# Kernel optimization log

Measured on AMD Instinct MI355X. Metric: run time of the kernel, lower is better.

## Reference

```python
import jax, jax.numpy as jnp
import numpy as np

N, IN_DIM, H1, H2, LIN, MAX_INDEX = 16384, 64, 256, 256, 64, 256


def _init_layer(key, out_dim, in_dim):
    # mimic kaiming_uniform(a=sqrt(5)) + uniform bias bound = 1/sqrt(fan_in)
    kW, kb = jax.random.split(key)
    bound_w = 1.0 / np.sqrt(in_dim)  # gain*sqrt(3/fan_in) with a=sqrt(5) -> 1/sqrt(fan_in)
    W = jax.random.uniform(kW, (MAX_INDEX, out_dim, in_dim), jnp.float32, -bound_w, bound_w)
    b = jax.random.uniform(kb, (MAX_INDEX, out_dim), jnp.float32, -bound_w, bound_w)
    return W, b


def setup_inputs() -> dict:
    key = jax.random.key(0)
    kx, ki, k1, k2, k3 = jax.random.split(key, 5)
    x = jax.random.normal(kx, (N, IN_DIM), jnp.float32)
    ind = jax.random.randint(ki, (N,), 0, MAX_INDEX, jnp.int64 if jax.config.jax_enable_x64 else jnp.int32)
    W1, b1 = _init_layer(k1, H1, IN_DIM)
    W2, b2 = _init_layer(k2, H2, H1)
    Wl, bl = _init_layer(k3, LIN, H2)
    return {"x": x, "ind": ind, "W1": W1, "b1": b1, "W2": W2, "b2": b2, "Wl": Wl, "bl": bl}


def _index_linear(x, ind, W, b):
    # per-row expert weight gather then row-wise matvec: out[n] = W[ind[n]] @ x[n] + b[ind[n]]
    return jnp.einsum('noi,ni->no', W[ind], x) + b[ind]


def reference(x, ind, W1, b1, W2, b2, Wl, bl):
    h = jnp.tanh(_index_linear(x, ind, W1, b1))
    h = jnp.tanh(_index_linear(h, ind, W2, b2))
    return _index_linear(h, ind, Wl, bl)
```

## Files before the change

kernel.cpp:

```cpp
#include <hip/hip_runtime.h>
#include <math.h>

#define NROWS   16384
#define IN_DIM  64
#define HID     256
#define OUT_DIM 64
#define NEXP    256
#define MT      64
#define HP      264

typedef __attribute__((ext_vector_type(8))) short short8;
typedef __attribute__((ext_vector_type(4))) float f32x4;
typedef __attribute__((ext_vector_type(4))) unsigned uint4v;
typedef __attribute__((ext_vector_type(2))) unsigned uint2v;


__global__ __launch_bounds__(1024) void prep_k(const int* __restrict__ ind,
                                               int* __restrict__ rows,
                                               int* __restrict__ offsets) {
  __shared__ int hist[NEXP];
  __shared__ int scan[NEXP];
  __shared__ int cur[NEXP];
  int t = threadIdx.x;
  if (t < NEXP) hist[t] = 0;
  __syncthreads();
  for (int n = t; n < NROWS; n += 1024) atomicAdd(&hist[ind[n]], 1);
  __syncthreads();
  if (t < NEXP) scan[t] = hist[t];
  __syncthreads();
  for (int d = 1; d < NEXP; d <<= 1) {
    int v = (t < NEXP && t >= d) ? scan[t - d] : 0;
    __syncthreads();
    if (t < NEXP) scan[t] += v;
    __syncthreads();
  }
  if (t < NEXP) {
    int exc = scan[t] - hist[t];
    offsets[t] = exc;
    cur[t] = exc;
    if (t == NEXP - 1) offsets[NEXP] = scan[t];
  }
  __syncthreads();
  for (int n = t; n < NROWS; n += 1024) {
    int p = atomicAdd(&cur[ind[n]], 1);
    rows[p] = n;
  }
}


__device__ __forceinline__ unsigned bf16_rn(float f) {
  unsigned u = __builtin_bit_cast(unsigned, f);
  unsigned r = 0x7fffu + ((u >> 16) & 1u);
  return (u + r) >> 16;
}

__device__ __forceinline__ unsigned pk2(float a, float b) {
  return bf16_rn(a) | (bf16_rn(b) << 16);
}

__device__ __forceinline__ short8 cvt8(f32x4 w0, f32x4 w1) {
  uint4v u;
  u.x = pk2(w0.x, w0.y);
  u.y = pk2(w0.z, w0.w);
  u.z = pk2(w1.x, w1.y);
  u.w = pk2(w1.z, w1.w);
  return __builtin_bit_cast(short8, u);
}

__device__ __forceinline__ float fast_tanh(float v) {
  float e = __expf(2.f * v);
  return 1.f - 2.f * __builtin_amdgcn_rcpf(e + 1.f);
}

template <int K, int NMT>
__device__ __forceinline__ void layer_mm(const float* __restrict__ Wp,
                                         const float* __restrict__ bp,
                                         const unsigned short* Hin,
                                         int l15, int q, f32x4 (&acc)[NMT][4]) {
#pragma unroll
  for (int mt = 0; mt < NMT; mt++) {
    f32x4 bv = *(const f32x4*)(bp + mt * 16 + q * 4);
#pragma unroll
    for (int nt = 0; nt < 4; nt++) acc[mt][nt] = bv;
  }
  const float* wr[NMT];
#pragma unroll
  for (int mt = 0; mt < NMT; mt++)
    wr[mt] = Wp + (size_t)(mt * 16 + l15) * K + q * 8;

#pragma unroll 2
  for (int ks = 0; ks < K / 32; ks++) {
    short8 bfr[4];
#pragma unroll
    for (int nt = 0; nt < 4; nt++)
      bfr[nt] = *(const short8*)&Hin[(nt * 16 + l15) * HP + ks * 32 + q * 8];
#pragma unroll
    for (int mt = 0; mt < NMT; mt++) {
      f32x4 w0 = *(const f32x4*)(wr[mt] + ks * 32);
      f32x4 w1 = *(const f32x4*)(wr[mt] + ks * 32 + 4);
      short8 a = cvt8(w0, w1);
#pragma unroll
      for (int nt = 0; nt < 4; nt++)
        acc[mt][nt] =
            __builtin_amdgcn_mfma_f32_16x16x32_bf16(a, bfr[nt], acc[mt][nt], 0, 0, 0);
    }
  }
}

__device__ __forceinline__ void write_h(f32x4 (&acc)[4][4], unsigned short* H,
                                        int w, int l15, int q) {
#pragma unroll
  for (int mt = 0; mt < 4; mt++)
#pragma unroll
    for (int nt = 0; nt < 4; nt++) {
      uint2v v;
      v.x = pk2(fast_tanh(acc[mt][nt].x), fast_tanh(acc[mt][nt].y));
      v.y = pk2(fast_tanh(acc[mt][nt].z), fast_tanh(acc[mt][nt].w));
      *(uint2v*)&H[(nt * 16 + l15) * HP + w * 64 + mt * 16 + q * 4] = v;
    }
}


__global__ __launch_bounds__(256, 2) void mlp_k(
    const float* __restrict__ x,
    const float* __restrict__ W1, const float* __restrict__ b1,
    const float* __restrict__ W2, const float* __restrict__ b2,
    const float* __restrict__ Wl, const float* __restrict__ bl,
    const int* __restrict__ rows, const int* __restrict__ offsets,
    float* __restrict__ out) {
  __shared__ __align__(16) unsigned short H[MT * HP];

  const int t = threadIdx.x;
  const int w = t >> 6;
  const int l15 = t & 15;
  const int q = (t >> 4) & 3;
  const int e = blockIdx.x >> 1;
  const int j = blockIdx.x & 1;
  const int beg = offsets[e];
  const int cnt = offsets[e + 1] - beg;

  const float* W1e = W1 + (size_t)e * HID * IN_DIM + (size_t)(w * 64) * IN_DIM;
  const float* W2e = W2 + (size_t)e * HID * HID + (size_t)(w * 64) * HID;
  const float* Wle = Wl + (size_t)e * OUT_DIM * HID + (size_t)(w * 16) * HID;
  const float* b1e = b1 + e * HID + w * 64;
  const float* b2e = b2 + e * HID + w * 64;
  const float* ble = bl + e * OUT_DIM + w * 16;

  const int sm = t >> 2;
  const int sc = (t & 3) * 16;

  for (int mt0 = j * MT; mt0 < cnt; mt0 += 2 * MT) {
    __syncthreads();
    {
      int gm = mt0 + sm;
      bool val = gm < cnt;
      int r = val ? rows[beg + gm] : 0;
      const float* xr = x + (size_t)r * IN_DIM + sc;
      uint4v u0, u1;
      if (val) {
        f32x4 a0 = *(const f32x4*)(xr);
        f32x4 a1 = *(const f32x4*)(xr + 4);
        f32x4 a2 = *(const f32x4*)(xr + 8);
        f32x4 a3 = *(const f32x4*)(xr + 12);
        u0.x = pk2(a0.x, a0.y); u0.y = pk2(a0.z, a0.w);
        u0.z = pk2(a1.x, a1.y); u0.w = pk2(a1.z, a1.w);
        u1.x = pk2(a2.x, a2.y); u1.y = pk2(a2.z, a2.w);
        u1.z = pk2(a3.x, a3.y); u1.w = pk2(a3.z, a3.w);
      } else {
        u0 = (uint4v){0, 0, 0, 0};
        u1 = (uint4v){0, 0, 0, 0};
      }
      *(uint4v*)&H[sm * HP + sc] = u0;
      *(uint4v*)&H[sm * HP + sc + 8] = u1;
    }
    __syncthreads();

    {
      f32x4 acc[4][4];
      layer_mm<IN_DIM, 4>(W1e, b1e, H, l15, q, acc);
      __syncthreads();
      write_h(acc, H, w, l15, q);
    }
    __syncthreads();

    {
      f32x4 acc[4][4];
      layer_mm<HID, 4>(W2e, b2e, H, l15, q, acc);
      __syncthreads();
      write_h(acc, H, w, l15, q);
    }
    __syncthreads();

    {
      f32x4 acc[1][4];
      layer_mm<HID, 1>(Wle, ble, H, l15, q, acc);
#pragma unroll
      for (int nt = 0; nt < 4; nt++) {
        int gm = mt0 + nt * 16 + l15;
        if (gm < cnt) {
          int r = rows[beg + gm];
          *(f32x4*)(out + (size_t)r * OUT_DIM + w * 16 + q * 4) = acc[0][nt];
        }
      }
    }
  }
}


extern "C" void kernel_launch(void* const* d_in, const int* in_sizes, int n_in,
                              void* d_out, int out_size, void* d_ws, size_t ws_size,
                              hipStream_t stream) {
  const float* x   = (const float*)d_in[0];
  const int*   ind = (const int*)d_in[1];
  const float* W1  = (const float*)d_in[2];
  const float* b1  = (const float*)d_in[3];
  const float* W2  = (const float*)d_in[4];
  const float* b2  = (const float*)d_in[5];
  const float* Wl  = (const float*)d_in[6];
  const float* bl  = (const float*)d_in[7];
  float* out = (float*)d_out;

  int* offsets = (int*)d_ws;
  int* rows    = (int*)d_ws + 260;

  prep_k<<<1, 1024, 0, stream>>>(ind, rows, offsets);
  mlp_k<<<NEXP * 2, 256, 0, stream>>>(x, W1, b1, W2, b2, Wl, bl, rows, offsets, out);
}
```

Measured before the change: 170.7 us.

## Shrink row tile to 32, prefetch weights, truncate weight bf16 conversion

Halves the per-block row tile from 64 to 32, so experts with about 64 rows get both blocks busy instead of one idling. Weight loads are software-prefetched one k-step ahead with a fully unrolled loop, weights are converted to bf16 by truncation instead of manual rounding, and activations use the HIP bf16 intrinsic. Blocks are reordered so the two halves of one expert are 256 apart in launch order. The trade-off is that each block now reloads the full expert weights for half as many rows, the prefetch raises register use, and truncating weights adds some error.

```diff
diff --git a/kernel.cpp b/kernel.cpp
--- a/kernel.cpp
+++ b/kernel.cpp
@@ -1,4 +1,5 @@
 #include <hip/hip_runtime.h>
+#include <hip/hip_bf16.h>
 #include <math.h>
 
 #define NROWS   16384
@@ -6,7 +7,7 @@
 #define HID     256
 #define OUT_DIM 64
 #define NEXP    256
-#define MT      64
+#define MT      32
 #define HP      264
 
 typedef __attribute__((ext_vector_type(8))) short short8;
@@ -48,22 +49,25 @@
 }
 
 
-__device__ __forceinline__ unsigned bf16_rn(float f) {
-  unsigned u = __builtin_bit_cast(unsigned, f);
-  unsigned r = 0x7fffu + ((u >> 16) & 1u);
-  return (u + r) >> 16;
-}
-
-__device__ __forceinline__ unsigned pk2(float a, float b) {
-  return bf16_rn(a) | (bf16_rn(b) << 16);
-}
-
-__device__ __forceinline__ short8 cvt8(f32x4 w0, f32x4 w1) {
+__device__ __forceinline__ unsigned pk2_trunc(float a, float b) {
+  unsigned ua = __builtin_bit_cast(unsigned, a);
+  unsigned ub = __builtin_bit_cast(unsigned, b);
+  return (ub & 0xffff0000u) | (ua >> 16);
+}
+
+__device__ __forceinline__ unsigned pk2_rn(float a, float b) {
+  __hip_bfloat162 h = __float22bfloat162_rn(float2{a, b});
+  unsigned r;
+  __builtin_memcpy(&r, &h, 4);
+  return r;
+}
+
+__device__ __forceinline__ short8 cvt8w(f32x4 w0, f32x4 w1) {
   uint4v u;
-  u.x = pk2(w0.x, w0.y);
-  u.y = pk2(w0.z, w0.w);
-  u.z = pk2(w1.x, w1.y);
-  u.w = pk2(w1.z, w1.w);
+  u.x = pk2_trunc(w0.x, w0.y);
+  u.y = pk2_trunc(w0.z, w0.w);
+  u.z = pk2_trunc(w1.x, w1.y);
+  u.w = pk2_trunc(w1.z, w1.w);
   return __builtin_bit_cast(short8, u);
 }
 
@@ -72,50 +76,67 @@
   return 1.f - 2.f * __builtin_amdgcn_rcpf(e + 1.f);
 }
 
-template <int K, int NMT>
+template <int K, int NMT, int NNT>
 __device__ __forceinline__ void layer_mm(const float* __restrict__ Wp,
                                          const float* __restrict__ bp,
                                          const unsigned short* Hin,
-                                         int l15, int q, f32x4 (&acc)[NMT][4]) {
+                                         int l15, int q, f32x4 (&acc)[NMT][NNT]) {
 #pragma unroll
   for (int mt = 0; mt < NMT; mt++) {
     f32x4 bv = *(const f32x4*)(bp + mt * 16 + q * 4);
 #pragma unroll
-    for (int nt = 0; nt < 4; nt++) acc[mt][nt] = bv;
+    for (int nt = 0; nt < NNT; nt++) acc[mt][nt] = bv;
   }
   const float* wr[NMT];
 #pragma unroll
   for (int mt = 0; mt < NMT; mt++)
     wr[mt] = Wp + (size_t)(mt * 16 + l15) * K + q * 8;
 
-#pragma unroll 2
-  for (int ks = 0; ks < K / 32; ks++) {
-    short8 bfr[4];
-#pragma unroll
-    for (int nt = 0; nt < 4; nt++)
+  constexpr int KS = K / 32;
+  f32x4 wcur[NMT][2], wnxt[NMT][2];
+#pragma unroll
+  for (int mt = 0; mt < NMT; mt++) {
+    wcur[mt][0] = *(const f32x4*)(wr[mt]);
+    wcur[mt][1] = *(const f32x4*)(wr[mt] + 4);
+  }
+#pragma unroll
+  for (int ks = 0; ks < KS; ks++) {
+    int kn = (ks + 1 < KS) ? (ks + 1) * 32 : 0;
+#pragma unroll
+    for (int mt = 0; mt < NMT; mt++) {
+      wnxt[mt][0] = *(const f32x4*)(wr[mt] + kn);
+      wnxt[mt][1] = *(const f32x4*)(wr[mt] + kn + 4);
+    }
+    short8 bfr[NNT];
+#pragma unroll
+    for (int nt = 0; nt < NNT; nt++)
       bfr[nt] = *(const short8*)&Hin[(nt * 16 + l15) * HP + ks * 32 + q * 8];
 #pragma unroll
     for (int mt = 0; mt < NMT; mt++) {
-      f32x4 w0 = *(const f32x4*)(wr[mt] + ks * 32);
-      f32x4 w1 = *(const f32x4*)(wr[mt] + ks * 32 + 4);
-      short8 a = cvt8(w0, w1);
-#pragma unroll
-      for (int nt = 0; nt < 4; nt++)
+      short8 a = cvt8w(wcur[mt][0], wcur[mt][1]);
+#pragma unroll
+      for (int nt = 0; nt < NNT; nt++)
         acc[mt][nt] =
             __builtin_amdgcn_mfma_f32_16x16x32_bf16(a, bfr[nt], acc[mt][nt], 0, 0, 0);
     }
-  }
-}
-
-__device__ __forceinline__ void write_h(f32x4 (&acc)[4][4], unsigned short* H,
+#pragma unroll
+    for (int mt = 0; mt < NMT; mt++) {
+      wcur[mt][0] = wnxt[mt][0];
+      wcur[mt][1] = wnxt[mt][1];
+    }
+  }
+}
+
+template <int NNT>
+__device__ __forceinline__ void write_h(f32x4 (&acc)[4][NNT], unsigned short* H,
                                         int w, int l15, int q) {
 #pragma unroll
   for (int mt = 0; mt < 4; mt++)
 #pragma unroll
-    for (int nt = 0; nt < 4; nt++) {
+    for (int nt = 0; nt < NNT; nt++) {
       uint2v v;
-      v.x = pk2(fast_tanh(acc[mt][nt].x), fast_tanh(acc[mt][nt].y));
-      v.y = pk2(fast_tanh(acc[mt][nt].z), fast_tanh(acc[mt][nt].w));
+      v.x = pk2_rn(fast_tanh(acc[mt][nt].x), fast_tanh(acc[mt][nt].y));
+      v.y = pk2_rn(fast_tanh(acc[mt][nt].z), fast_tanh(acc[mt][nt].w));
       *(uint2v*)&H[(nt * 16 + l15) * HP + w * 64 + mt * 16 + q * 4] = v;
     }
 }
@@ -134,8 +155,8 @@
   const int w = t >> 6;
   const int l15 = t & 15;
   const int q = (t >> 4) & 3;
-  const int e = blockIdx.x >> 1;
-  const int j = blockIdx.x & 1;
+  const int e = blockIdx.x & 255;
+  const int j = blockIdx.x >> 8;
   const int beg = offsets[e];
   const int cnt = offsets[e + 1] - beg;
 
@@ -146,8 +167,8 @@
   const float* b2e = b2 + e * HID + w * 64;
   const float* ble = bl + e * OUT_DIM + w * 16;
 
-  const int sm = t >> 2;
-  const int sc = (t & 3) * 16;
+  const int sm = t >> 3;
+  const int sc = (t & 7) * 8;
 
   for (int mt0 = j * MT; mt0 < cnt; mt0 += 2 * MT) {
     __syncthreads();
@@ -156,46 +177,40 @@
       bool val = gm < cnt;
       int r = val ? rows[beg + gm] : 0;
       const float* xr = x + (size_t)r * IN_DIM + sc;
-      uint4v u0, u1;
+      uint4v u;
       if (val) {
         f32x4 a0 = *(const f32x4*)(xr);
         f32x4 a1 = *(const f32x4*)(xr + 4);
-        f32x4 a2 = *(const f32x4*)(xr + 8);
-        f32x4 a3 = *(const f32x4*)(xr + 12);
-        u0.x = pk2(a0.x, a0.y); u0.y = pk2(a0.z, a0.w);
-        u0.z = pk2(a1.x, a1.y); u0.w = pk2(a1.z, a1.w);
-        u1.x = pk2(a2.x, a2.y); u1.y = pk2(a2.z, a2.w);
-        u1.z = pk2(a3.x, a3.y); u1.w = pk2(a3.z, a3.w);
+        u.x = pk2_rn(a0.x, a0.y); u.y = pk2_rn(a0.z, a0.w);
+        u.z = pk2_rn(a1.x, a1.y); u.w = pk2_rn(a1.z, a1.w);
       } else {
-        u0 = (uint4v){0, 0, 0, 0};
-        u1 = (uint4v){0, 0, 0, 0};
+        u = (uint4v){0, 0, 0, 0};
       }
-      *(uint4v*)&H[sm * HP + sc] = u0;
-      *(uint4v*)&H[sm * HP + sc + 8] = u1;
-    }
-    __syncthreads();
-
-    {
-      f32x4 acc[4][4];
-      layer_mm<IN_DIM, 4>(W1e, b1e, H, l15, q, acc);
+      *(uint4v*)&H[sm * HP + sc] = u;
+    }
+    __syncthreads();
+
+    {
+      f32x4 acc[4][2];
+      layer_mm<IN_DIM, 4, 2>(W1e, b1e, H, l15, q, acc);
       __syncthreads();
-      write_h(acc, H, w, l15, q);
-    }
-    __syncthreads();
-
-    {
-      f32x4 acc[4][4];
-      layer_mm<HID, 4>(W2e, b2e, H, l15, q, acc);
+      write_h<2>(acc, H, w, l15, q);
+    }
+    __syncthreads();
+
+    {
+      f32x4 acc[4][2];
+      layer_mm<HID, 4, 2>(W2e, b2e, H, l15, q, acc);
       __syncthreads();
-      write_h(acc, H, w, l15, q);
-    }
-    __syncthreads();
-
-    {
-      f32x4 acc[1][4];
-      layer_mm<HID, 1>(Wle, ble, H, l15, q, acc);
-#pragma unroll
-      for (int nt = 0; nt < 4; nt++) {
+      write_h<2>(acc, H, w, l15, q);
+    }
+    __syncthreads();
+
+    {
+      f32x4 acc[1][2];
+      layer_mm<HID, 1, 2>(Wle, ble, H, l15, q, acc);
+#pragma unroll
+      for (int nt = 0; nt < 2; nt++) {
         int gm = mt0 + nt * 16 + l15;
         if (gm < cnt) {
           int r = rows[beg + gm];
```

After: 187.3 us. 9.7% more time.
